# Kernel tuning notes

Measured on AMD Instinct MI355X. Metric: run time of the kernel, lower is better.

The kernel has to match this reference:

```python
import jax, jax.numpy as jnp
import numpy as np

KH, KW = 2, 3          # kernel_size of the masked (shifted) conv
CW = KW // 2           # width padding for order 'A'
B, C, H, W = 8, 32, 256, 256
HID = 64


def _wn(v, g):
    # weight normalization: w = g * v / ||v||, norm over (in, kh, kw) per out channel
    norm = jnp.sqrt(jnp.sum(v * v, axis=(1, 2, 3), keepdims=True))
    return v * (g[:, None, None, None] / norm)


def _conv(x, w, b):
    y = jax.lax.conv_general_dilated(
        x, w, window_strides=(1, 1), padding='VALID',
        dimension_numbers=('NCHW', 'OIHW', 'NCHW'))
    return y + b[None, :, None, None]


def setup_inputs() -> dict:
    key = jax.random.key(0)
    ks = jax.random.split(key, 4)
    x = jax.random.normal(ks[0], (B, C, H, W), dtype=jnp.float32)
    v1 = jax.random.normal(ks[1], (HID, C, KH, KW), dtype=jnp.float32) * 0.05
    g1 = jnp.ones((HID,), dtype=jnp.float32)
    b1 = jnp.zeros((HID,), dtype=jnp.float32)
    v2 = jax.random.normal(ks[2], (2 * C, HID, 1, 1), dtype=jnp.float32) * 0.05
    g2 = jnp.ones((2 * C,), dtype=jnp.float32)
    b2 = jnp.zeros((2 * C,), dtype=jnp.float32)
    return {"x": x, "v1": v1, "g1": g1, "b1": b1, "v2": v2, "g2": g2, "b2": b2}


def reference(x, v1, g1, b1, v2, g2, b2):
    # ShiftedConv2d, order 'A': pad KH rows on top, CW cols each side, drop last
    # row, then VALID conv -> output at row h only sees input rows h-KH..h-1.
    xs = jnp.pad(x, ((0, 0), (0, 0), (KH, 0), (CW, CW)))[:, :, :-1, :]
    h = _conv(xs, _wn(v1, g1), b1)                 # [B, HID, H, W]
    h = jax.nn.elu(h)
    ms = _conv(h, _wn(v2, g2), b2)                 # [B, 2C, H, W]
    mu, log_scale = jnp.split(ms, 2, axis=1)
    scale = jax.nn.sigmoid(log_scale + 2.0)
    out = x * scale + mu                           # affine flow
    logdet = jnp.sum(jnp.log(scale).reshape(x.shape[0], -1), axis=1)  # [B]
    return out, logdet
```

## Files before the change

kernel.cpp:

```cpp
#include <hip/hip_runtime.h>
#include <hip/hip_bf16.h>
#include <math.h>

#define B_   8
#define C_   32
#define H_   256
#define W_   256
#define NPIX (B_*C_*H_*W_)

typedef __attribute__((ext_vector_type(8))) short short8;
typedef __attribute__((ext_vector_type(4))) float f32x4;
typedef __attribute__((ext_vector_type(2))) float f32x2;

static __device__ __forceinline__ short f2bf(float f) {
    union { __hip_bfloat16 h; short s; } u; u.h = __float2bfloat16(f); return u.s;
}

__global__ __launch_bounds__(64) void prep_kernel(
    const float* __restrict__ v1, const float* __restrict__ g1,
    const float* __restrict__ v2, const float* __restrict__ g2,
    short* __restrict__ w1b, short* __restrict__ w2b,
    float* __restrict__ logdet)
{
    const int t   = threadIdx.x;
    const int bid = blockIdx.x;
    if (bid < 64) {
        const int o = bid;
        float a0 = v1[o*192 + t];
        float a1 = v1[o*192 + t + 64];
        float a2 = v1[o*192 + t + 128];
        float s  = a0*a0 + a1*a1 + a2*a2;
        #pragma unroll
        for (int m = 32; m >= 1; m >>= 1) s += __shfl_xor(s, m, 64);
        const float inv = g1[o] / sqrtf(s);
        const int e0 = t, e1 = t + 64, e2 = t + 128;
        w1b[o*192 + (e0%6)*32 + e0/6] = f2bf(a0*inv);
        w1b[o*192 + (e1%6)*32 + e1/6] = f2bf(a1*inv);
        w1b[o*192 + (e2%6)*32 + e2/6] = f2bf(a2*inv);
        if (bid == 0 && t < B_) logdet[t] = 0.f;
    } else {
        const int j = bid - 64;
        float a = v2[j*64 + t];
        float s = a*a;
        #pragma unroll
        for (int m = 32; m >= 1; m >>= 1) s += __shfl_xor(s, m, 64);
        const float inv = g2[j] / sqrtf(s);
        const int mt = t >> 4, r = t & 15;
        const int slot = (mt >> 1)*32 + ((r >> 2) << 3) + ((mt & 1) << 2) + (r & 3);
        w2b[j*64 + slot] = f2bf(a*inv);
    }
}

__global__ __launch_bounds__(256) void flow_kernel(
    const float* __restrict__ x,
    const short* __restrict__ w1b, const short* __restrict__ w2b,
    const float* __restrict__ b1,  const float* __restrict__ b2,
    float* __restrict__ out, float* __restrict__ logdet)
{
    __shared__ int ldsI[8192];
    __shared__ float red4[4];

    const int bi0 = blockIdx.x;
    const int bi  = (bi0 & 7) * 256 + (bi0 >> 3);
    const int b   = bi >> 8;
    const int h   = bi & 255;
    const int tid  = threadIdx.x;
    const int l    = tid & 63;
    const int wv   = tid >> 6;
    const int lrow = l & 15;
    const int q    = l >> 4;

    const float* xb = x + (size_t)b * (C_*H_*W_);

    {
        const int r   = tid >> 7;
        const int w0  = (tid & 127) << 1;
        const int hr  = h - 2 + r;
        const int swz = (w0 >> 1) & 3;
        const int base = r*4096 + w0*16;
        if (hr >= 0) {
            const float* pr = xb + (size_t)hr * W_ + w0;
            #pragma unroll
            for (int cp = 0; cp < 16; ++cp) {
                f32x2 a0 = *(const f32x2*)(pr + (size_t)(2*cp  ) * (H_*W_));
                f32x2 a1 = *(const f32x2*)(pr + (size_t)(2*cp+1) * (H_*W_));
                const int lo = (int)(unsigned short)f2bf(a0[0]) | ((int)(unsigned short)f2bf(a1[0]) << 16);
                const int hi = (int)(unsigned short)f2bf(a0[1]) | ((int)(unsigned short)f2bf(a1[1]) << 16);
                const int o  = ((cp >> 2) ^ swz)*4 + (cp & 3);
                ldsI[base + o]      = lo;
                ldsI[base + 16 + o] = hi;
            }
        } else {
            #pragma unroll
            for (int cp = 0; cp < 16; ++cp) {
                const int o = ((cp >> 2) ^ swz)*4 + (cp & 3);
                ldsI[base + o] = 0; ldsI[base + 16 + o] = 0;
            }
        }
    }
    __syncthreads();

    f32x4 acc1[4][4];
    #pragma unroll
    for (int mt = 0; mt < 4; ++mt) {
        const f32x4 bv = *(const f32x4*)(b1 + mt*16 + 4*q);
        #pragma unroll
        for (int nt = 0; nt < 4; ++nt) acc1[mt][nt] = bv;
    }

    const short8 zero8 = {0,0,0,0,0,0,0,0};
    #pragma unroll
    for (int tap = 0; tap < 6; ++tap) {
        const int r  = tap / 3;
        const int dw = (tap % 3) - 1;
        short8 wf[4];
        #pragma unroll
        for (int mt = 0; mt < 4; ++mt)
            wf[mt] = *(const short8*)(w1b + (mt*16 + lrow)*192 + tap*32 + q*8);
        #pragma unroll
        for (int nt = 0; nt < 4; ++nt) {
            const int pxo = wv*64 + nt*16 + lrow;
            const int px  = pxo + dw;
            const int pxc = px < 0 ? 0 : (px > 255 ? 255 : px);
            const int byteoff = r*16384 + pxc*64 + ((q ^ ((pxc >> 1) & 3)) << 4);
            short8 xf = *(const short8*)((const char*)ldsI + byteoff);
            if (px != pxc) xf = zero8;
            #pragma unroll
            for (int mt = 0; mt < 4; ++mt)
                acc1[mt][nt] = __builtin_amdgcn_mfma_f32_16x16x32_bf16(
                                   wf[mt], xf, acc1[mt][nt], 0, 0, 0);
        }
    }

    #pragma unroll
    for (int mt = 0; mt < 4; ++mt)
        #pragma unroll
        for (int nt = 0; nt < 4; ++nt)
            #pragma unroll
            for (int rg = 0; rg < 4; ++rg) {
                const float v = acc1[mt][nt][rg];
                acc1[mt][nt][rg] = v > 0.f ? v : (__expf(v) - 1.f);
            }

    short8 a2f[2][4];
    #pragma unroll
    for (int kt = 0; kt < 2; ++kt)
        #pragma unroll
        for (int mt2 = 0; mt2 < 4; ++mt2)
            a2f[kt][mt2] = *(const short8*)(w2b + (mt2*16 + lrow)*64 + kt*32 + q*8);

    f32x4 acc2[4][4];
    #pragma unroll
    for (int nt = 0; nt < 4; ++nt) {
        short8 bf0, bf1;
        #pragma unroll
        for (int rg = 0; rg < 4; ++rg) {
            bf0[rg]     = f2bf(acc1[0][nt][rg]);
            bf0[rg + 4] = f2bf(acc1[1][nt][rg]);
            bf1[rg]     = f2bf(acc1[2][nt][rg]);
            bf1[rg + 4] = f2bf(acc1[3][nt][rg]);
        }
        #pragma unroll
        for (int mt2 = 0; mt2 < 4; ++mt2) {
            f32x4 t0 = __builtin_amdgcn_mfma_f32_16x16x32_bf16(
                           a2f[0][mt2], bf0, (f32x4){0.f,0.f,0.f,0.f}, 0, 0, 0);
            acc2[mt2][nt] = __builtin_amdgcn_mfma_f32_16x16x32_bf16(
                           a2f[1][mt2], bf1, t0, 0, 0, 0);
        }
    }

    f32x4 b2m[2], b2s[2];
    #pragma unroll
    for (int mt2 = 0; mt2 < 2; ++mt2) {
        b2m[mt2] = *(const f32x4*)(b2 + mt2*16 + 4*q);
        b2s[mt2] = *(const f32x4*)(b2 + 32 + mt2*16 + 4*q);
    }

    float ldsum = 0.f;
    float* ob = out + (size_t)b * (C_*H_*W_);
    #pragma unroll
    for (int nt = 0; nt < 4; ++nt) {
        const int px = wv*64 + nt*16 + lrow;
        const int colbase = h*W_ + px;
        #pragma unroll
        for (int mt2 = 0; mt2 < 2; ++mt2)
            #pragma unroll
            for (int rg = 0; rg < 4; ++rg) {
                const int j = mt2*16 + 4*q + rg;
                const float mu = acc2[mt2][nt][rg]     + b2m[mt2][rg];
                const float z  = acc2[mt2 + 2][nt][rg] + b2s[mt2][rg] + 2.f;
                const float sc = 1.f / (1.f + __expf(-z));
                ldsum += __logf(sc);
                const size_t idx = (size_t)j * (H_*W_) + colbase;
                ob[idx] = xb[idx] * sc + mu;
            }
    }

    #pragma unroll
    for (int m = 32; m >= 1; m >>= 1) ldsum += __shfl_xor(ldsum, m, 64);
    if (l == 0) red4[wv] = ldsum;
    __syncthreads();
    if (tid == 0) atomicAdd(&logdet[b], red4[0] + red4[1] + red4[2] + red4[3]);
}

extern "C" void kernel_launch(void* const* d_in, const int* in_sizes, int n_in,
                              void* d_out, int out_size, void* d_ws, size_t ws_size,
                              hipStream_t stream)
{
    const float* x  = (const float*)d_in[0];
    const float* v1 = (const float*)d_in[1];
    const float* g1 = (const float*)d_in[2];
    const float* b1 = (const float*)d_in[3];
    const float* v2 = (const float*)d_in[4];
    const float* g2 = (const float*)d_in[5];
    const float* b2 = (const float*)d_in[6];

    float* out    = (float*)d_out;
    float* logdet = out + NPIX;

    short* w1b = (short*)d_ws;
    short* w2b = w1b + 12288;

    prep_kernel<<<128, 64, 0, stream>>>(v1, g1, v2, g2, w1b, w2b, logdet);
    flow_kernel<<<B_ * H_, 256, 0, stream>>>(x, w1b, w2b, b1, b2, out, logdet);
}
```

Baseline: 71.20 us.

## Process two output rows per block with rolling LDS row buffer

Each block now computes two consecutive output rows, reusing the shared input row between them through a double-slot LDS ring. This avoids re-staging that row and halves the block count. Staging switches to 16-byte loads of four pixels across eight channels, with a matching LDS swizzle. Part of the next row's loads are issued before the first row's compute to hide latency. It adds occupancy hints and extra barriers, and the grid has half as many blocks.

```diff
diff --git a/kernel.cpp b/kernel.cpp
--- a/kernel.cpp
+++ b/kernel.cpp
@@ -10,10 +10,12 @@
 
 typedef __attribute__((ext_vector_type(8))) short short8;
 typedef __attribute__((ext_vector_type(4))) float f32x4;
-typedef __attribute__((ext_vector_type(2))) float f32x2;
 
 static __device__ __forceinline__ short f2bf(float f) {
     union { __hip_bfloat16 h; short s; } u; u.h = __float2bfloat16(f); return u.s;
+}
+static __device__ __forceinline__ int packbf(float a, float b) {
+    return (int)(unsigned short)f2bf(a) | ((int)(unsigned short)f2bf(b) << 16);
 }
 
 __global__ __launch_bounds__(64) void prep_kernel(
@@ -51,7 +53,7 @@
     }
 }
 
-__global__ __launch_bounds__(256) void flow_kernel(
+__global__ __launch_bounds__(256, 4) void flow_kernel(
     const float* __restrict__ x,
     const short* __restrict__ w1b, const short* __restrict__ w2b,
     const float* __restrict__ b1,  const float* __restrict__ b2,
@@ -61,140 +63,172 @@
     __shared__ float red4[4];
 
     const int bi0 = blockIdx.x;
-    const int bi  = (bi0 & 7) * 256 + (bi0 >> 3);
-    const int b   = bi >> 8;
-    const int h   = bi & 255;
+    const int b   = bi0 & 7;
+    const int h0  = (bi0 >> 3) << 1;
+
     const int tid  = threadIdx.x;
     const int l    = tid & 63;
     const int wv   = tid >> 6;
     const int lrow = l & 15;
     const int q    = l >> 4;
 
+    const int w4 = (tid & 63) << 2;
+    const int cg = tid >> 6;
+    const int c8 = cg << 3;
+
     const float* xb = x + (size_t)b * (C_*H_*W_);
-
-    {
-        const int r   = tid >> 7;
-        const int w0  = (tid & 127) << 1;
-        const int hr  = h - 2 + r;
-        const int swz = (w0 >> 1) & 3;
-        const int base = r*4096 + w0*16;
+    float* ob       = out + (size_t)b * (C_*H_*W_);
+
+    auto stage_write = [&](int slotbase, const f32x4* qv) {
+        #pragma unroll
+        for (int p = 0; p < 4; ++p) {
+            const int w  = w4 + p;
+            const int sw = (w >> 2) & 3;
+            int4 d;
+            d.x = packbf(qv[0][p], qv[1][p]);
+            d.y = packbf(qv[2][p], qv[3][p]);
+            d.z = packbf(qv[4][p], qv[5][p]);
+            d.w = packbf(qv[6][p], qv[7][p]);
+            *(int4*)&ldsI[slotbase + w*16 + ((cg ^ sw) << 2)] = d;
+        }
+    };
+    auto stage_row = [&](int hr, int slotbase) {
         if (hr >= 0) {
-            const float* pr = xb + (size_t)hr * W_ + w0;
-            #pragma unroll
-            for (int cp = 0; cp < 16; ++cp) {
-                f32x2 a0 = *(const f32x2*)(pr + (size_t)(2*cp  ) * (H_*W_));
-                f32x2 a1 = *(const f32x2*)(pr + (size_t)(2*cp+1) * (H_*W_));
-                const int lo = (int)(unsigned short)f2bf(a0[0]) | ((int)(unsigned short)f2bf(a1[0]) << 16);
-                const int hi = (int)(unsigned short)f2bf(a0[1]) | ((int)(unsigned short)f2bf(a1[1]) << 16);
-                const int o  = ((cp >> 2) ^ swz)*4 + (cp & 3);
-                ldsI[base + o]      = lo;
-                ldsI[base + 16 + o] = hi;
-            }
+            f32x4 qv[8];
+            #pragma unroll
+            for (int j = 0; j < 8; ++j)
+                qv[j] = *(const f32x4*)(xb + (size_t)(c8 + j)*(H_*W_) + (size_t)hr*W_ + w4);
+            stage_write(slotbase, qv);
         } else {
             #pragma unroll
-            for (int cp = 0; cp < 16; ++cp) {
-                const int o = ((cp >> 2) ^ swz)*4 + (cp & 3);
-                ldsI[base + o] = 0; ldsI[base + 16 + o] = 0;
-            }
-        }
-    }
-    __syncthreads();
-
-    f32x4 acc1[4][4];
+            for (int p = 0; p < 4; ++p) {
+                const int w  = w4 + p;
+                const int sw = (w >> 2) & 3;
+                *(int4*)&ldsI[slotbase + w*16 + ((cg ^ sw) << 2)] = (int4){0,0,0,0};
+            }
+        }
+    };
+
+    auto compute_row = [&](int h) -> float {
+        const int sb0 = ( h      & 1) << 14;
+        const int sb1 = ((h + 1) & 1) << 14;
+
+        f32x4 acc1[4][4];
+        #pragma unroll
+        for (int mt = 0; mt < 4; ++mt) {
+            const f32x4 bv = *(const f32x4*)(b1 + mt*16 + 4*q);
+            #pragma unroll
+            for (int nt = 0; nt < 4; ++nt) acc1[mt][nt] = bv;
+        }
+
+        const short8 zero8 = {0,0,0,0,0,0,0,0};
+        #pragma unroll
+        for (int tap = 0; tap < 6; ++tap) {
+            const int rb = (tap < 3) ? sb0 : sb1;
+            const int dw = (tap % 3) - 1;
+            short8 wf[4];
+            #pragma unroll
+            for (int mt = 0; mt < 4; ++mt)
+                wf[mt] = *(const short8*)(w1b + (mt*16 + lrow)*192 + tap*32 + q*8);
+            #pragma unroll
+            for (int nt = 0; nt < 4; ++nt) {
+                const int pxo = wv*64 + nt*16 + lrow;
+                const int px  = pxo + dw;
+                const int pxc = px < 0 ? 0 : (px > 255 ? 255 : px);
+                const int byteoff = rb + pxc*64 + ((q ^ ((pxc >> 2) & 3)) << 4);
+                short8 xf = *(const short8*)((const char*)ldsI + byteoff);
+                if (px != pxc) xf = zero8;
+                #pragma unroll
+                for (int mt = 0; mt < 4; ++mt)
+                    acc1[mt][nt] = __builtin_amdgcn_mfma_f32_16x16x32_bf16(
+                                       wf[mt], xf, acc1[mt][nt], 0, 0, 0);
+            }
+        }
+
+        #pragma unroll
+        for (int mt = 0; mt < 4; ++mt)
+            #pragma unroll
+            for (int nt = 0; nt < 4; ++nt)
+                #pragma unroll
+                for (int rg = 0; rg < 4; ++rg) {
+                    const float v = acc1[mt][nt][rg];
+                    acc1[mt][nt][rg] = v > 0.f ? v : (__expf(v) - 1.f);
+                }
+
+        short8 a2f[2][4];
+        #pragma unroll
+        for (int kt = 0; kt < 2; ++kt)
+            #pragma unroll
+            for (int mt2 = 0; mt2 < 4; ++mt2)
+                a2f[kt][mt2] = *(const short8*)(w2b + (mt2*16 + lrow)*64 + kt*32 + q*8);
+
+        f32x4 acc2[4][4];
+        #pragma unroll
+        for (int nt = 0; nt < 4; ++nt) {
+            short8 bf0, bf1;
+            #pragma unroll
+            for (int rg = 0; rg < 4; ++rg) {
+                bf0[rg]     = f2bf(acc1[0][nt][rg]);
+                bf0[rg + 4] = f2bf(acc1[1][nt][rg]);
+                bf1[rg]     = f2bf(acc1[2][nt][rg]);
+                bf1[rg + 4] = f2bf(acc1[3][nt][rg]);
+            }
+            #pragma unroll
+            for (int mt2 = 0; mt2 < 4; ++mt2) {
+                f32x4 t0 = __builtin_amdgcn_mfma_f32_16x16x32_bf16(
+                               a2f[0][mt2], bf0, (f32x4){0.f,0.f,0.f,0.f}, 0, 0, 0);
+                acc2[mt2][nt] = __builtin_amdgcn_mfma_f32_16x16x32_bf16(
+                               a2f[1][mt2], bf1, t0, 0, 0, 0);
+            }
+        }
+
+        f32x4 b2m[2], b2s[2];
+        #pragma unroll
+        for (int mt2 = 0; mt2 < 2; ++mt2) {
+            b2m[mt2] = *(const f32x4*)(b2 + mt2*16 + 4*q);
+            b2s[mt2] = *(const f32x4*)(b2 + 32 + mt2*16 + 4*q);
+        }
+
+        float ldsum = 0.f;
+        #pragma unroll
+        for (int nt = 0; nt < 4; ++nt) {
+            const int px = wv*64 + nt*16 + lrow;
+            const int colbase = h*W_ + px;
+            #pragma unroll
+            for (int mt2 = 0; mt2 < 2; ++mt2)
+                #pragma unroll
+                for (int rg = 0; rg < 4; ++rg) {
+                    const int j = mt2*16 + 4*q + rg;
+                    const float mu = acc2[mt2][nt][rg]     + b2m[mt2][rg];
+                    const float z  = acc2[mt2 + 2][nt][rg] + b2s[mt2][rg] + 2.f;
+                    const float sc = 1.f / (1.f + __expf(-z));
+                    ldsum += __logf(sc);
+                    const size_t idx = (size_t)j * (H_*W_) + colbase;
+                    ob[idx] = xb[idx] * sc + mu;
+                }
+        }
+        return ldsum;
+    };
+
+    stage_row(h0 - 2, 0);
+    stage_row(h0 - 1, 4096);
+    __syncthreads();
+
+    f32x4 qv[8];
     #pragma unroll
-    for (int mt = 0; mt < 4; ++mt) {
-        const f32x4 bv = *(const f32x4*)(b1 + mt*16 + 4*q);
-        #pragma unroll
-        for (int nt = 0; nt < 4; ++nt) acc1[mt][nt] = bv;
-    }
-
-    const short8 zero8 = {0,0,0,0,0,0,0,0};
+    for (int j = 0; j < 4; ++j)
+        qv[j] = *(const f32x4*)(xb + (size_t)(c8 + j)*(H_*W_) + (size_t)h0*W_ + w4);
+
+    float ldsum = compute_row(h0);
+    __syncthreads();
+
     #pragma unroll
-    for (int tap = 0; tap < 6; ++tap) {
-        const int r  = tap / 3;
-        const int dw = (tap % 3) - 1;
-        short8 wf[4];
-        #pragma unroll
-        for (int mt = 0; mt < 4; ++mt)
-            wf[mt] = *(const short8*)(w1b + (mt*16 + lrow)*192 + tap*32 + q*8);
-        #pragma unroll
-        for (int nt = 0; nt < 4; ++nt) {
-            const int pxo = wv*64 + nt*16 + lrow;
-            const int px  = pxo + dw;
-            const int pxc = px < 0 ? 0 : (px > 255 ? 255 : px);
-            const int byteoff = r*16384 + pxc*64 + ((q ^ ((pxc >> 1) & 3)) << 4);
-            short8 xf = *(const short8*)((const char*)ldsI + byteoff);
-            if (px != pxc) xf = zero8;
-            #pragma unroll
-            for (int mt = 0; mt < 4; ++mt)
-                acc1[mt][nt] = __builtin_amdgcn_mfma_f32_16x16x32_bf16(
-                                   wf[mt], xf, acc1[mt][nt], 0, 0, 0);
-        }
-    }
-
-    #pragma unroll
-    for (int mt = 0; mt < 4; ++mt)
-        #pragma unroll
-        for (int nt = 0; nt < 4; ++nt)
-            #pragma unroll
-            for (int rg = 0; rg < 4; ++rg) {
-                const float v = acc1[mt][nt][rg];
-                acc1[mt][nt][rg] = v > 0.f ? v : (__expf(v) - 1.f);
-            }
-
-    short8 a2f[2][4];
-    #pragma unroll
-    for (int kt = 0; kt < 2; ++kt)
-        #pragma unroll
-        for (int mt2 = 0; mt2 < 4; ++mt2)
-            a2f[kt][mt2] = *(const short8*)(w2b + (mt2*16 + lrow)*64 + kt*32 + q*8);
-
-    f32x4 acc2[4][4];
-    #pragma unroll
-    for (int nt = 0; nt < 4; ++nt) {
-        short8 bf0, bf1;
-        #pragma unroll
-        for (int rg = 0; rg < 4; ++rg) {
-            bf0[rg]     = f2bf(acc1[0][nt][rg]);
-            bf0[rg + 4] = f2bf(acc1[1][nt][rg]);
-            bf1[rg]     = f2bf(acc1[2][nt][rg]);
-            bf1[rg + 4] = f2bf(acc1[3][nt][rg]);
-        }
-        #pragma unroll
-        for (int mt2 = 0; mt2 < 4; ++mt2) {
-            f32x4 t0 = __builtin_amdgcn_mfma_f32_16x16x32_bf16(
-                           a2f[0][mt2], bf0, (f32x4){0.f,0.f,0.f,0.f}, 0, 0, 0);
-            acc2[mt2][nt] = __builtin_amdgcn_mfma_f32_16x16x32_bf16(
-                           a2f[1][mt2], bf1, t0, 0, 0, 0);
-        }
-    }
-
-    f32x4 b2m[2], b2s[2];
-    #pragma unroll
-    for (int mt2 = 0; mt2 < 2; ++mt2) {
-        b2m[mt2] = *(const f32x4*)(b2 + mt2*16 + 4*q);
-        b2s[mt2] = *(const f32x4*)(b2 + 32 + mt2*16 + 4*q);
-    }
-
-    float ldsum = 0.f;
-    float* ob = out + (size_t)b * (C_*H_*W_);
-    #pragma unroll
-    for (int nt = 0; nt < 4; ++nt) {
-        const int px = wv*64 + nt*16 + lrow;
-        const int colbase = h*W_ + px;
-        #pragma unroll
-        for (int mt2 = 0; mt2 < 2; ++mt2)
-            #pragma unroll
-            for (int rg = 0; rg < 4; ++rg) {
-                const int j = mt2*16 + 4*q + rg;
-                const float mu = acc2[mt2][nt][rg]     + b2m[mt2][rg];
-                const float z  = acc2[mt2 + 2][nt][rg] + b2s[mt2][rg] + 2.f;
-                const float sc = 1.f / (1.f + __expf(-z));
-                ldsum += __logf(sc);
-                const size_t idx = (size_t)j * (H_*W_) + colbase;
-                ob[idx] = xb[idx] * sc + mu;
-            }
-    }
+    for (int j = 4; j < 8; ++j)
+        qv[j] = *(const f32x4*)(xb + (size_t)(c8 + j)*(H_*W_) + (size_t)h0*W_ + w4);
+    stage_write(0, qv);
+    __syncthreads();
+
+    ldsum += compute_row(h0 + 1);
 
     #pragma unroll
     for (int m = 32; m >= 1; m >>= 1) ldsum += __shfl_xor(ldsum, m, 64);
@@ -222,5 +256,5 @@
     short* w2b = w1b + 12288;
 
     prep_kernel<<<128, 64, 0, stream>>>(v1, g1, v2, g2, w1b, w2b, logdet);
-    flow_kernel<<<B_ * H_, 256, 0, stream>>>(x, w1b, w2b, b1, b2, out, logdet);
-}
+    flow_kernel<<<B_ * H_ / 2, 256, 0, stream>>>(x, w1b, w2b, b1, b2, out, logdet);
+}
```

Measured after the change: 99.38 us. +39.6%, slower.

## Widen x staging loads, pad LDS rows, and drop block-level logdet sync

Applied to the files above, without the earlier changes.

The staging of the two input rows into LDS now uses 16-byte float4 loads over 8 channels and writes 16-byte packed bf16 vectors, replacing 8-byte loads with scalar int stores. Each LDS row gets zeroed halo columns on both sides so the conv taps need no clamping or select. The final logdet reduction issues one atomic per wave instead of a shared-memory reduction behind a second __syncthreads. In exchange there are more global atomics, a changed swizzle pattern, and more registers held during staging.

```diff
diff --git a/kernel.cpp b/kernel.cpp
--- a/kernel.cpp
+++ b/kernel.cpp
@@ -8,12 +8,18 @@
 #define W_   256
 #define NPIX (B_*C_*H_*W_)
 
+#define PW    260
+#define ROWDW (PW*16)
+#define ROWB  (ROWDW*4)
+
 typedef __attribute__((ext_vector_type(8))) short short8;
 typedef __attribute__((ext_vector_type(4))) float f32x4;
-typedef __attribute__((ext_vector_type(2))) float f32x2;
 
 static __device__ __forceinline__ short f2bf(float f) {
     union { __hip_bfloat16 h; short s; } u; u.h = __float2bfloat16(f); return u.s;
+}
+static __device__ __forceinline__ int packbf(float a, float b) {
+    return (int)(unsigned short)f2bf(a) | ((int)(unsigned short)f2bf(b) << 16);
 }
 
 __global__ __launch_bounds__(64) void prep_kernel(
@@ -57,13 +63,13 @@
     const float* __restrict__ b1,  const float* __restrict__ b2,
     float* __restrict__ out, float* __restrict__ logdet)
 {
-    __shared__ int ldsI[8192];
-    __shared__ float red4[4];
+    __shared__ int ldsI[2*ROWDW];
 
     const int bi0 = blockIdx.x;
     const int bi  = (bi0 & 7) * 256 + (bi0 >> 3);
     const int b   = bi >> 8;
     const int h   = bi & 255;
+
     const int tid  = threadIdx.x;
     const int l    = tid & 63;
     const int wv   = tid >> 6;
@@ -71,31 +77,49 @@
     const int q    = l >> 4;
 
     const float* xb = x + (size_t)b * (C_*H_*W_);
+    float* ob       = out + (size_t)b * (C_*H_*W_);
 
     {
-        const int r   = tid >> 7;
-        const int w0  = (tid & 127) << 1;
-        const int hr  = h - 2 + r;
-        const int swz = (w0 >> 1) & 3;
-        const int base = r*4096 + w0*16;
-        if (hr >= 0) {
-            const float* pr = xb + (size_t)hr * W_ + w0;
-            #pragma unroll
-            for (int cp = 0; cp < 16; ++cp) {
-                f32x2 a0 = *(const f32x2*)(pr + (size_t)(2*cp  ) * (H_*W_));
-                f32x2 a1 = *(const f32x2*)(pr + (size_t)(2*cp+1) * (H_*W_));
-                const int lo = (int)(unsigned short)f2bf(a0[0]) | ((int)(unsigned short)f2bf(a1[0]) << 16);
-                const int hi = (int)(unsigned short)f2bf(a0[1]) | ((int)(unsigned short)f2bf(a1[1]) << 16);
-                const int o  = ((cp >> 2) ^ swz)*4 + (cp & 3);
-                ldsI[base + o]      = lo;
-                ldsI[base + 16 + o] = hi;
+        const int r  = tid >> 7;
+        const int hr = h - 2 + r;
+        const int u0 = tid & 127;
+        #pragma unroll
+        for (int ui = 0; ui < 2; ++ui) {
+            const int unit = u0 + ui*128;
+            const int qd   = unit & 63;
+            const int cg   = unit >> 6;
+            const int w4   = qd << 2;
+            const int c8   = cg << 3;
+            if (hr >= 0) {
+                f32x4 qv[8];
+                #pragma unroll
+                for (int j = 0; j < 8; ++j)
+                    qv[j] = *(const f32x4*)(xb + (size_t)(c8 + j)*(H_*W_) + (size_t)hr*W_ + w4);
+                #pragma unroll
+                for (int pp = 0; pp < 4; ++pp) {
+                    const int p  = w4 + pp + 1;
+                    const int sw = (p >> 2) & 3;
+                    int4 d;
+                    d.x = packbf(qv[0][pp], qv[1][pp]);
+                    d.y = packbf(qv[2][pp], qv[3][pp]);
+                    d.z = packbf(qv[4][pp], qv[5][pp]);
+                    d.w = packbf(qv[6][pp], qv[7][pp]);
+                    *(int4*)&ldsI[r*ROWDW + p*16 + ((cg ^ sw) << 2)] = d;
+                }
+            } else {
+                #pragma unroll
+                for (int pp = 0; pp < 4; ++pp) {
+                    const int p  = w4 + pp + 1;
+                    const int sw = (p >> 2) & 3;
+                    *(int4*)&ldsI[r*ROWDW + p*16 + ((cg ^ sw) << 2)] = (int4){0,0,0,0};
+                }
             }
-        } else {
-            #pragma unroll
-            for (int cp = 0; cp < 16; ++cp) {
-                const int o = ((cp >> 2) ^ swz)*4 + (cp & 3);
-                ldsI[base + o] = 0; ldsI[base + 16 + o] = 0;
-            }
+        }
+        if (tid < 16) {
+            const int rz  = tid >> 3;
+            const int pz  = (tid >> 2) & 1 ? 257 : 0;
+            const int seg = tid & 3;
+            *(int4*)&ldsI[rz*ROWDW + pz*16 + seg*4] = (int4){0,0,0,0};
         }
     }
     __syncthreads();
@@ -108,10 +132,9 @@
         for (int nt = 0; nt < 4; ++nt) acc1[mt][nt] = bv;
     }
 
-    const short8 zero8 = {0,0,0,0,0,0,0,0};
     #pragma unroll
     for (int tap = 0; tap < 6; ++tap) {
-        const int r  = tap / 3;
+        const int rb = (tap < 3) ? 0 : ROWB;
         const int dw = (tap % 3) - 1;
         short8 wf[4];
         #pragma unroll
@@ -119,12 +142,9 @@
             wf[mt] = *(const short8*)(w1b + (mt*16 + lrow)*192 + tap*32 + q*8);
         #pragma unroll
         for (int nt = 0; nt < 4; ++nt) {
-            const int pxo = wv*64 + nt*16 + lrow;
-            const int px  = pxo + dw;
-            const int pxc = px < 0 ? 0 : (px > 255 ? 255 : px);
-            const int byteoff = r*16384 + pxc*64 + ((q ^ ((pxc >> 1) & 3)) << 4);
-            short8 xf = *(const short8*)((const char*)ldsI + byteoff);
-            if (px != pxc) xf = zero8;
+            const int p = wv*64 + nt*16 + lrow + dw + 1;
+            const int byteoff = rb + p*64 + ((q ^ ((p >> 2) & 3)) << 4);
+            const short8 xf = *(const short8*)((const char*)ldsI + byteoff);
             #pragma unroll
             for (int mt = 0; mt < 4; ++mt)
                 acc1[mt][nt] = __builtin_amdgcn_mfma_f32_16x16x32_bf16(
@@ -177,7 +197,6 @@
     }
 
     float ldsum = 0.f;
-    float* ob = out + (size_t)b * (C_*H_*W_);
     #pragma unroll
     for (int nt = 0; nt < 4; ++nt) {
         const int px = wv*64 + nt*16 + lrow;
@@ -186,11 +205,11 @@
         for (int mt2 = 0; mt2 < 2; ++mt2)
             #pragma unroll
             for (int rg = 0; rg < 4; ++rg) {
-                const int j = mt2*16 + 4*q + rg;
                 const float mu = acc2[mt2][nt][rg]     + b2m[mt2][rg];
                 const float z  = acc2[mt2 + 2][nt][rg] + b2s[mt2][rg] + 2.f;
                 const float sc = 1.f / (1.f + __expf(-z));
                 ldsum += __logf(sc);
+                const int j = mt2*16 + 4*q + rg;
                 const size_t idx = (size_t)j * (H_*W_) + colbase;
                 ob[idx] = xb[idx] * sc + mu;
             }
@@ -198,9 +217,7 @@
 
     #pragma unroll
     for (int m = 32; m >= 1; m >>= 1) ldsum += __shfl_xor(ldsum, m, 64);
-    if (l == 0) red4[wv] = ldsum;
-    __syncthreads();
-    if (tid == 0) atomicAdd(&logdet[b], red4[0] + red4[1] + red4[2] + red4[3]);
+    if (l == 0) atomicAdd(&logdet[b], ldsum);
 }
 
 extern "C" void kernel_launch(void* const* d_in, const int* in_sizes, int n_in,
```

Result: slower. 140.5 us (+97.3%).
